# Kernel tuning notes

Measured on AMD Instinct MI355X. Metric: run time of the kernel, lower is better.

Reference implementation:

```python
import jax, jax.numpy as jnp
import numpy as np

EMBED_DIM = 768
NUM_HEADS = 12
HEAD_DIM = EMBED_DIM // NUM_HEADS


def setup_inputs() -> dict:
    key = jax.random.key(0)
    ks = jax.random.split(key, 9)
    B, N, C = 4, 2048, EMBED_DIM
    s = 1.0 / np.sqrt(C)
    x = jax.random.normal(ks[0], (B, N, C), dtype=jnp.float32)
    Wq = jax.random.normal(ks[1], (C, C), dtype=jnp.float32) * s
    bq = jnp.zeros((C,), dtype=jnp.float32)
    Wk = jax.random.normal(ks[2], (C, C), dtype=jnp.float32) * s
    bk = jnp.zeros((C,), dtype=jnp.float32)
    Wv = jax.random.normal(ks[3], (C, C), dtype=jnp.float32) * s
    bv = jnp.zeros((C,), dtype=jnp.float32)
    Wo = jax.random.normal(ks[4], (C, C), dtype=jnp.float32) * s
    bo = jnp.zeros((C,), dtype=jnp.float32)
    return {"x": x, "Wq": Wq, "bq": bq, "Wk": Wk, "bk": bk,
            "Wv": Wv, "bv": bv, "Wo": Wo, "bo": bo}


def reference(x, Wq, bq, Wk, bk, Wv, bv, Wo, bo):
    # Dropout in eval mode (identity), matching module.eval().
    B, N, C = x.shape
    H, D = NUM_HEADS, HEAD_DIM
    scale = D ** -0.5

    def split_heads(t):  # [B,N,C] -> [B,H,N,D]
        return t.reshape(B, N, H, D).transpose(0, 2, 1, 3)

    q = split_heads(x @ Wq.T + bq)
    k = split_heads(x @ Wk.T + bk)
    v = split_heads(x @ Wv.T + bv)

    attn = jnp.einsum('bhnd,bhmd->bhnm', q, k) * scale  # [B,H,N,N]
    attn = jax.nn.softmax(attn, axis=-1)
    out = jnp.einsum('bhnm,bhmd->bhnd', attn, v)        # [B,H,N,D]
    out = out.transpose(0, 2, 1, 3).reshape(B, N, C)
    return out @ Wo.T + bo
```

## Files before the change

### kernel.cpp

```cpp
#include <hip/hip_runtime.h>
#include <math.h>

#define CDIM 768
#define NHEADS 12
#define HDIM 64
#define BATCH 4
#define SEQ 2048
#define MTOT (BATCH*SEQ)
#define NQKV (3*CDIM)
#define QROWS 128

typedef __attribute__((ext_vector_type(8))) short bf16x8;
typedef __attribute__((ext_vector_type(4))) float f32x4;
typedef unsigned short u16;

#define ASYNC16(gsrc, ldst) \
  __builtin_amdgcn_global_load_lds((const __attribute__((address_space(1))) void*)(gsrc), \
                                   (__attribute__((address_space(3))) void*)(ldst), 16, 0, 0)

__device__ inline u16 f2b(float x) {
    unsigned int u = __float_as_uint(x);
    return (u16)((u + 0x7fffu + ((u >> 16) & 1u)) >> 16);
}
__device__ inline u16 f2b_hu(float x) {
    return (u16)((__float_as_uint(x) + 0x8000u) >> 16);
}

__global__ void f2bf_kern(const float* __restrict__ in, u16* __restrict__ out, int n)
{
    int i = (blockIdx.x * 256 + threadIdx.x) * 4;
    if (i >= n) return;
    float4 v = *(const float4*)(in + i);
    ushort4 o;
    o.x = f2b(v.x); o.y = f2b(v.y); o.z = f2b(v.z); o.w = f2b(v.w);
    *(ushort4*)(out + i) = o;
}

__global__ void castw_kern(const float* __restrict__ Wq, const float* __restrict__ Wk,
                           const float* __restrict__ Wv, const float* __restrict__ Wo,
                           u16* __restrict__ wqkv, u16* __restrict__ wob)
{
    int z = blockIdx.y;
    const float* src = (z == 0) ? Wq : (z == 1) ? Wk : (z == 2) ? Wv : Wo;
    u16* dst = (z == 3) ? wob : wqkv + (size_t)z * CDIM * CDIM;
    int i = (blockIdx.x * 256 + threadIdx.x) * 4;
    float4 v = *(const float4*)(src + i);
    ushort4 o;
    o.x = f2b(v.x); o.y = f2b(v.y); o.z = f2b(v.z); o.w = f2b(v.w);
    *(ushort4*)(dst + i) = o;
}

__global__ void catbias_kern(const float* __restrict__ bq, const float* __restrict__ bk,
                             const float* __restrict__ bv, float* __restrict__ out)
{
    int i = blockIdx.x * 256 + threadIdx.x;
    if (i < CDIM) out[i] = bq[i];
    else if (i < 2*CDIM) out[i] = bk[i - CDIM];
    else if (i < 3*CDIM) out[i] = bv[i - 2*CDIM];
}

template<int OUTF32>
__global__ __launch_bounds__(256)
void gemm_bf16(const u16* __restrict__ A, const u16* __restrict__ B,
               const float* __restrict__ bias, void* __restrict__ Y,
               int N, int K, int qn, float qscale)
{
    __shared__ __align__(16) u16 As[128*64];
    __shared__ __align__(16) u16 Bs[128*64];
    const int tid = threadIdx.x;
    const int m0 = blockIdx.y * 128, n0 = blockIdx.x * 128;
    const int wid = tid >> 6, lane = tid & 63;
    const int wm = (wid & 1) * 64, wn = (wid >> 1) * 64;
    const int l15 = lane & 15, quad = lane >> 4;

    f32x4 acc[4][4];
    #pragma unroll
    for (int i = 0; i < 4; ++i)
        #pragma unroll
        for (int j = 0; j < 4; ++j)
            #pragma unroll
            for (int r = 0; r < 4; ++r) acc[i][j][r] = 0.f;

    for (int k0 = 0; k0 < K; k0 += 64) {
        __syncthreads();
        #pragma unroll
        for (int r = 0; r < 4; ++r) {
            int li = r*256 + tid;
            int row = li >> 3, c = li & 7;
            int gc = c ^ (row & 7);
            ASYNC16(A + (size_t)(m0 + row) * K + k0 + gc*8, &As[li*8]);
            ASYNC16(B + (size_t)(n0 + row) * K + k0 + gc*8, &Bs[li*8]);
        }
        __syncthreads();
        #pragma unroll
        for (int kk = 0; kk < 2; ++kk) {
            bf16x8 a[4], b[4];
            #pragma unroll
            for (int i = 0; i < 4; ++i) {
                int m = wm + i*16 + l15;
                int ca = (kk*4 + quad) ^ (m & 7);
                a[i] = *(const bf16x8*)&As[m*64 + ca*8];
                int n = wn + i*16 + l15;
                int cb = (kk*4 + quad) ^ (n & 7);
                b[i] = *(const bf16x8*)&Bs[n*64 + cb*8];
            }
            #pragma unroll
            for (int i = 0; i < 4; ++i)
                #pragma unroll
                for (int j = 0; j < 4; ++j)
                    acc[i][j] = __builtin_amdgcn_mfma_f32_16x16x32_bf16(a[i], b[j], acc[i][j], 0, 0, 0);
        }
    }

    #pragma unroll
    for (int i = 0; i < 4; ++i) {
        #pragma unroll
        for (int j = 0; j < 4; ++j) {
            int gn = n0 + wn + j*16 + l15;
            float bv = bias[gn];
            float sc = (gn < qn) ? qscale : 1.0f;
            #pragma unroll
            for (int r = 0; r < 4; ++r) {
                int gm = m0 + wm + i*16 + quad*4 + r;
                float v = (acc[i][j][r] + bv) * sc;
                if (OUTF32) ((float*)Y)[(size_t)gm * N + gn] = v;
                else        ((u16*)Y)[(size_t)gm * N + gn] = f2b(v);
            }
        }
    }
}

__global__ __launch_bounds__(256)
void transpose_v(const u16* __restrict__ QKV, u16* __restrict__ Vt)
{
    __shared__ __align__(16) u16 Vs[64*72];
    const int tid = threadIdx.x;
    const int nt = blockIdx.x, bh = blockIdx.y;
    const int b = bh / NHEADS, h = bh % NHEADS;
    const u16* src = QKV + ((size_t)(b*SEQ + nt*64)) * NQKV + 2*CDIM + h*HDIM;
    #pragma unroll
    for (int rep = 0; rep < 2; ++rep) {
        int li = rep*256 + tid, r = li >> 3, c = li & 7;
        *(uint4*)&Vs[r*72 + c*8] = *(const uint4*)(src + (size_t)r * NQKV + c*8);
    }
    __syncthreads();
    u16* dst = Vt + ((size_t)bh * 64) * SEQ + nt*64;
    #pragma unroll
    for (int rep = 0; rep < 2; ++rep) {
        int li = rep*256 + tid, d = li >> 3, c = li & 7;
        u16 tmp[8];
        #pragma unroll
        for (int j = 0; j < 8; ++j) tmp[j] = Vs[(c*8 + j)*72 + d];
        *(uint4*)(dst + (size_t)d * SEQ + c*8) = *(const uint4*)tmp;
    }
}

__global__ __launch_bounds__(256, 3)
void attn_mfma(const u16* __restrict__ QK, const u16* __restrict__ Vt,
               u16* __restrict__ Oa)
{
    __shared__ __align__(16) u16 Ps[QROWS*72];
    __shared__ __align__(16) u16 Ks[2][64*64];
    __shared__ __align__(16) u16 Vs[2][64*64];

    const int tid = threadIdx.x;
    const int wid = tid >> 6, lane = tid & 63;
    const int l15 = lane & 15, quad = lane >> 4;
    const int qt = blockIdx.x, bh = blockIdx.y;
    const int b = bh / NHEADS, h = bh % NHEADS;

    const u16* Qg  = QK + ((size_t)(b*SEQ + qt*QROWS)) * NQKV + h*HDIM;
    const u16* Kg0 = QK + ((size_t)(b*SEQ)) * NQKV + CDIM + h*HDIM;
    const u16* Vg0 = Vt + (size_t)bh * HDIM * SEQ;

    #pragma unroll
    for (int r = 0; r < 4; ++r) {
        int li = r*256 + tid, row = li >> 3, c = li & 7, gc = c ^ (row & 7);
        ASYNC16(Qg + (size_t)row * NQKV + gc*8, &Ps[li*8]);
    }
    #pragma unroll
    for (int r = 0; r < 2; ++r) {
        int li = r*256 + tid, row = li >> 3, c = li & 7, gc = c ^ (row & 7);
        ASYNC16(Kg0 + (size_t)row * NQKV + gc*8, &Ks[0][li*8]);
        ASYNC16(Vg0 + (size_t)row * SEQ + gc*8, &Vs[0][li*8]);
    }
    __syncthreads();

    bf16x8 qf[2][2];
    #pragma unroll
    for (int mb = 0; mb < 2; ++mb)
        #pragma unroll
        for (int kk = 0; kk < 2; ++kk) {
            int m = wid*32 + mb*16 + l15;
            int c = (kk*4 + quad) ^ (m & 7);
            qf[mb][kk] = *(const bf16x8*)&Ps[m*64 + c*8];
        }
    __syncthreads();

    f32x4 o[2][4];
    #pragma unroll
    for (int mb = 0; mb < 2; ++mb)
        #pragma unroll
        for (int j = 0; j < 4; ++j)
            #pragma unroll
            for (int r = 0; r < 4; ++r) o[mb][j][r] = 0.f;
    float l_run[2][4] = {};

    for (int kt = 0; kt < SEQ/64; ++kt) {
        const int cb = kt & 1, nb = cb ^ 1;
        if (kt + 1 < SEQ/64) {
            #pragma unroll
            for (int r = 0; r < 2; ++r) {
                int li = r*256 + tid, row = li >> 3, c = li & 7, gc = c ^ (row & 7);
                ASYNC16(Kg0 + (size_t)((kt+1)*64 + row) * NQKV + gc*8, &Ks[nb][li*8]);
                ASYNC16(Vg0 + (size_t)row * SEQ + (kt+1)*64 + gc*8, &Vs[nb][li*8]);
            }
        }

        f32x4 s[2][4];
        #pragma unroll
        for (int mb = 0; mb < 2; ++mb)
            #pragma unroll
            for (int j = 0; j < 4; ++j)
                #pragma unroll
                for (int r = 0; r < 4; ++r) s[mb][j][r] = 0.f;
        #pragma unroll
        for (int kk = 0; kk < 2; ++kk) {
            bf16x8 bk[4];
            #pragma unroll
            for (int j = 0; j < 4; ++j) {
                int nk = j*16 + l15;
                int ck = (kk*4 + quad) ^ (nk & 7);
                bk[j] = *(const bf16x8*)&Ks[cb][nk*64 + ck*8];
            }
            #pragma unroll
            for (int mb = 0; mb < 2; ++mb)
                #pragma unroll
                for (int j = 0; j < 4; ++j)
                    s[mb][j] = __builtin_amdgcn_mfma_f32_16x16x32_bf16(qf[mb][kk], bk[j], s[mb][j], 0, 0, 0);
        }

        #pragma unroll
        for (int mb = 0; mb < 2; ++mb)
            #pragma unroll
            for (int j = 0; j < 4; ++j)
                #pragma unroll
                for (int r = 0; r < 4; ++r) {
                    float p = __expf(s[mb][j][r]);
                    l_run[mb][r] += p;
                    Ps[(wid*32 + mb*16 + quad*4 + r)*72 + j*16 + l15] = f2b_hu(p);
                }

        #pragma unroll
        for (int kk = 0; kk < 2; ++kk) {
            bf16x8 bv[4];
            #pragma unroll
            for (int j = 0; j < 4; ++j) {
                int nd = j*16 + l15;
                int cv = (kk*4 + quad) ^ (nd & 7);
                bv[j] = *(const bf16x8*)&Vs[cb][nd*64 + cv*8];
            }
            #pragma unroll
            for (int mb = 0; mb < 2; ++mb) {
                bf16x8 ap = *(const bf16x8*)&Ps[(wid*32 + mb*16 + l15)*72 + (kk*4 + quad)*8];
                #pragma unroll
                for (int j = 0; j < 4; ++j)
                    o[mb][j] = __builtin_amdgcn_mfma_f32_16x16x32_bf16(ap, bv[j], o[mb][j], 0, 0, 0);
            }
        }
        __syncthreads();
    }

    u16* Og = Oa + ((size_t)(b*SEQ + qt*QROWS)) * CDIM + h*HDIM;
    #pragma unroll
    for (int mb = 0; mb < 2; ++mb)
        #pragma unroll
        for (int r = 0; r < 4; ++r) {
            float l = l_run[mb][r];
            #pragma unroll
            for (int off = 1; off < 16; off <<= 1)
                l += __shfl_xor(l, off);
            float inv = 1.f / l;
            int row = wid*32 + mb*16 + quad*4 + r;
            #pragma unroll
            for (int j = 0; j < 4; ++j)
                Og[(size_t)row * CDIM + j*16 + l15] = f2b(o[mb][j][r] * inv);
        }
}

extern "C" void kernel_launch(void* const* d_in, const int* in_sizes, int n_in,
                              void* d_out, int out_size, void* d_ws, size_t ws_size,
                              hipStream_t stream)
{
    const float* x  = (const float*)d_in[0];
    const float* Wq = (const float*)d_in[1];
    const float* bq = (const float*)d_in[2];
    const float* Wk = (const float*)d_in[3];
    const float* bk = (const float*)d_in[4];
    const float* Wv = (const float*)d_in[5];
    const float* bv = (const float*)d_in[6];
    const float* Wo = (const float*)d_in[7];
    const float* bo = (const float*)d_in[8];

    unsigned char* ws = (unsigned char*)d_ws;
    u16* xb   = (u16*)ws;  ws += (size_t)MTOT * CDIM * 2;
    u16* wqkv = (u16*)ws;  ws += (size_t)NQKV * CDIM * 2;
    u16* wob  = (u16*)ws;  ws += (size_t)CDIM * CDIM * 2;
    float* bcat = (float*)ws; ws += (size_t)NQKV * 4;
    u16* qkv  = (u16*)ws;  ws += (size_t)MTOT * NQKV * 2;
    u16* vt   = (u16*)ws;  ws += (size_t)BATCH*NHEADS*HDIM*SEQ * 2;
    u16* ao   = (u16*)ws;

    f2bf_kern<<<MTOT*CDIM/1024, 256, 0, stream>>>(x, xb, MTOT*CDIM);
    castw_kern<<<dim3(CDIM*CDIM/1024, 4), 256, 0, stream>>>(Wq, Wk, Wv, Wo, wqkv, wob);
    catbias_kern<<<(NQKV+255)/256, 256, 0, stream>>>(bq, bk, bv, bcat);

    gemm_bf16<0><<<dim3(NQKV/128, MTOT/128), 256, 0, stream>>>(xb, wqkv, bcat, qkv, NQKV, CDIM, CDIM, 0.125f);
    transpose_v<<<dim3(SEQ/64, BATCH*NHEADS), 256, 0, stream>>>(qkv, vt);
    attn_mfma<<<dim3(SEQ/QROWS, BATCH*NHEADS), 256, 0, stream>>>(qkv, vt, ao);
    gemm_bf16<1><<<dim3(CDIM/128, MTOT/128), 256, 0, stream>>>(ao, wob, bo, (float*)d_out, CDIM, CDIM, 0, 1.0f);
}
```

Measured before the change: 251.8 us.

## Keep attention probabilities in registers via transposed QK^T MFMA

The score MFMA is computed as K·Q^T so each lane's accumulator layout matches the A-operand of a 16x16x16 bf16 MFMA. The exponentiated probabilities are then packed into bf16x4 fragments directly, with no round-trip through the shared Ps buffer. The row sums come from an extra MFMA against a ones vector, which replaces the per-lane accumulation and cross-lane shuffles. exp is replaced by exp2 with log2e folded into the Q scale, Q is loaded directly from global memory, and the Ps shared array is removed, freeing LDS for occupancy. The cost is a smaller-K MFMA for PV and narrower 8-byte V reads from LDS.

```diff
diff --git a/kernel.cpp b/kernel.cpp
--- a/kernel.cpp
+++ b/kernel.cpp
@@ -11,8 +11,10 @@
 #define QROWS 128
 
 typedef __attribute__((ext_vector_type(8))) short bf16x8;
+typedef __attribute__((ext_vector_type(4))) short bf16x4;
 typedef __attribute__((ext_vector_type(4))) float f32x4;
 typedef unsigned short u16;
+typedef unsigned int u32;
 
 #define ASYNC16(gsrc, ldst) \
   __builtin_amdgcn_global_load_lds((const __attribute__((address_space(1))) void*)(gsrc), \
@@ -22,9 +24,7 @@
     unsigned int u = __float_as_uint(x);
     return (u16)((u + 0x7fffu + ((u >> 16) & 1u)) >> 16);
 }
-__device__ inline u16 f2b_hu(float x) {
-    return (u16)((__float_as_uint(x) + 0x8000u) >> 16);
-}
+__device__ inline u32 prnd(float x) { return __float_as_uint(x) + 0x8000u; }
 
 __global__ void f2bf_kern(const float* __restrict__ in, u16* __restrict__ out, int n)
 {
@@ -159,7 +159,6 @@
 void attn_mfma(const u16* __restrict__ QK, const u16* __restrict__ Vt,
                u16* __restrict__ Oa)
 {
-    __shared__ __align__(16) u16 Ps[QROWS*72];
     __shared__ __align__(16) u16 Ks[2][64*64];
     __shared__ __align__(16) u16 Vs[2][64*64];
 
@@ -174,37 +173,34 @@
     const u16* Vg0 = Vt + (size_t)bh * HDIM * SEQ;
 
     #pragma unroll
-    for (int r = 0; r < 4; ++r) {
-        int li = r*256 + tid, row = li >> 3, c = li & 7, gc = c ^ (row & 7);
-        ASYNC16(Qg + (size_t)row * NQKV + gc*8, &Ps[li*8]);
-    }
-    #pragma unroll
     for (int r = 0; r < 2; ++r) {
         int li = r*256 + tid, row = li >> 3, c = li & 7, gc = c ^ (row & 7);
         ASYNC16(Kg0 + (size_t)row * NQKV + gc*8, &Ks[0][li*8]);
         ASYNC16(Vg0 + (size_t)row * SEQ + gc*8, &Vs[0][li*8]);
     }
+    bf16x8 qf[2][2];
+    #pragma unroll
+    for (int mb = 0; mb < 2; ++mb)
+        #pragma unroll
+        for (int kk = 0; kk < 2; ++kk)
+            qf[mb][kk] = *(const bf16x8*)(Qg + (size_t)(wid*32 + mb*16 + l15) * NQKV + kk*32 + quad*8);
+
+    const bf16x4 ONES = { (short)0x3F80, (short)0x3F80, (short)0x3F80, (short)0x3F80 };
+
+    f32x4 o[2][4];
+    #pragma unroll
+    for (int mb = 0; mb < 2; ++mb)
+        #pragma unroll
+        for (int j = 0; j < 4; ++j)
+            #pragma unroll
+            for (int r = 0; r < 4; ++r) o[mb][j][r] = 0.f;
+    f32x4 ll[2];
+    #pragma unroll
+    for (int mb = 0; mb < 2; ++mb)
+        #pragma unroll
+        for (int r = 0; r < 4; ++r) ll[mb][r] = 0.f;
+
     __syncthreads();
-
-    bf16x8 qf[2][2];
-    #pragma unroll
-    for (int mb = 0; mb < 2; ++mb)
-        #pragma unroll
-        for (int kk = 0; kk < 2; ++kk) {
-            int m = wid*32 + mb*16 + l15;
-            int c = (kk*4 + quad) ^ (m & 7);
-            qf[mb][kk] = *(const bf16x8*)&Ps[m*64 + c*8];
-        }
-    __syncthreads();
-
-    f32x4 o[2][4];
-    #pragma unroll
-    for (int mb = 0; mb < 2; ++mb)
-        #pragma unroll
-        for (int j = 0; j < 4; ++j)
-            #pragma unroll
-            for (int r = 0; r < 4; ++r) o[mb][j][r] = 0.f;
-    float l_run[2][4] = {};
 
     for (int kt = 0; kt < SEQ/64; ++kt) {
         const int cb = kt & 1, nb = cb ^ 1;
@@ -226,66 +222,62 @@
                 for (int r = 0; r < 4; ++r) s[mb][j][r] = 0.f;
         #pragma unroll
         for (int kk = 0; kk < 2; ++kk) {
-            bf16x8 bk[4];
             #pragma unroll
             for (int j = 0; j < 4; ++j) {
-                int nk = j*16 + l15;
-                int ck = (kk*4 + quad) ^ (nk & 7);
-                bk[j] = *(const bf16x8*)&Ks[cb][nk*64 + ck*8];
+                int kr = j*16 + l15;
+                int ck = (kk*4 + quad) ^ (kr & 7);
+                bf16x8 ak = *(const bf16x8*)&Ks[cb][kr*64 + ck*8];
+                #pragma unroll
+                for (int mb = 0; mb < 2; ++mb)
+                    s[mb][j] = __builtin_amdgcn_mfma_f32_16x16x32_bf16(ak, qf[mb][kk], s[mb][j], 0, 0, 0);
+            }
+        }
+
+        bf16x4 pf[2][4];
+        #pragma unroll
+        for (int mb = 0; mb < 2; ++mb)
+            #pragma unroll
+            for (int ks = 0; ks < 4; ++ks) {
+                u32 u0 = prnd(__builtin_amdgcn_exp2f(s[mb][ks][0]));
+                u32 u1 = prnd(__builtin_amdgcn_exp2f(s[mb][ks][1]));
+                u32 u2 = prnd(__builtin_amdgcn_exp2f(s[mb][ks][2]));
+                u32 u3 = prnd(__builtin_amdgcn_exp2f(s[mb][ks][3]));
+                union { uint2 u; bf16x4 v; } cst;
+                cst.u.x = __builtin_amdgcn_perm(u1, u0, 0x07060302u);
+                cst.u.y = __builtin_amdgcn_perm(u3, u2, 0x07060302u);
+                pf[mb][ks] = cst.v;
+            }
+
+        #pragma unroll
+        for (int ks = 0; ks < 4; ++ks) {
+            int seqoff = ks*16 + quad*4;
+            int chunk = (seqoff >> 3) ^ (l15 & 7);
+            #pragma unroll
+            for (int jd = 0; jd < 4; ++jd) {
+                bf16x4 vv = *(const bf16x4*)&Vs[cb][(jd*16 + l15)*64 + chunk*8 + (seqoff & 7)];
+                #pragma unroll
+                for (int mb = 0; mb < 2; ++mb)
+                    o[mb][jd] = __builtin_amdgcn_mfma_f32_16x16x16bf16_1k(pf[mb][ks], vv, o[mb][jd], 0, 0, 0);
             }
             #pragma unroll
             for (int mb = 0; mb < 2; ++mb)
-                #pragma unroll
-                for (int j = 0; j < 4; ++j)
-                    s[mb][j] = __builtin_amdgcn_mfma_f32_16x16x32_bf16(qf[mb][kk], bk[j], s[mb][j], 0, 0, 0);
-        }
-
-        #pragma unroll
-        for (int mb = 0; mb < 2; ++mb)
-            #pragma unroll
-            for (int j = 0; j < 4; ++j)
-                #pragma unroll
-                for (int r = 0; r < 4; ++r) {
-                    float p = __expf(s[mb][j][r]);
-                    l_run[mb][r] += p;
-                    Ps[(wid*32 + mb*16 + quad*4 + r)*72 + j*16 + l15] = f2b_hu(p);
-                }
-
-        #pragma unroll
-        for (int kk = 0; kk < 2; ++kk) {
-            bf16x8 bv[4];
-            #pragma unroll
-            for (int j = 0; j < 4; ++j) {
-                int nd = j*16 + l15;
-                int cv = (kk*4 + quad) ^ (nd & 7);
-                bv[j] = *(const bf16x8*)&Vs[cb][nd*64 + cv*8];
-            }
-            #pragma unroll
-            for (int mb = 0; mb < 2; ++mb) {
-                bf16x8 ap = *(const bf16x8*)&Ps[(wid*32 + mb*16 + l15)*72 + (kk*4 + quad)*8];
-                #pragma unroll
-                for (int j = 0; j < 4; ++j)
-                    o[mb][j] = __builtin_amdgcn_mfma_f32_16x16x32_bf16(ap, bv[j], o[mb][j], 0, 0, 0);
-            }
+                ll[mb] = __builtin_amdgcn_mfma_f32_16x16x16bf16_1k(pf[mb][ks], ONES, ll[mb], 0, 0, 0);
         }
         __syncthreads();
     }
 
     u16* Og = Oa + ((size_t)(b*SEQ + qt*QROWS)) * CDIM + h*HDIM;
     #pragma unroll
-    for (int mb = 0; mb < 2; ++mb)
+    for (int mb = 0; mb < 2; ++mb) {
         #pragma unroll
         for (int r = 0; r < 4; ++r) {
-            float l = l_run[mb][r];
-            #pragma unroll
-            for (int off = 1; off < 16; off <<= 1)
-                l += __shfl_xor(l, off);
-            float inv = 1.f / l;
+            float inv = 1.f / ll[mb][r];
             int row = wid*32 + mb*16 + quad*4 + r;
             #pragma unroll
-            for (int j = 0; j < 4; ++j)
-                Og[(size_t)row * CDIM + j*16 + l15] = f2b(o[mb][j][r] * inv);
-        }
+            for (int jd = 0; jd < 4; ++jd)
+                Og[(size_t)row * CDIM + jd*16 + l15] = f2b(o[mb][jd][r] * inv);
+        }
+    }
 }
 
 extern "C" void kernel_launch(void* const* d_in, const int* in_sizes, int n_in,
@@ -315,7 +307,7 @@
     castw_kern<<<dim3(CDIM*CDIM/1024, 4), 256, 0, stream>>>(Wq, Wk, Wv, Wo, wqkv, wob);
     catbias_kern<<<(NQKV+255)/256, 256, 0, stream>>>(bq, bk, bv, bcat);
 
-    gemm_bf16<0><<<dim3(NQKV/128, MTOT/128), 256, 0, stream>>>(xb, wqkv, bcat, qkv, NQKV, CDIM, CDIM, 0.125f);
+    gemm_bf16<0><<<dim3(NQKV/128, MTOT/128), 256, 0, stream>>>(xb, wqkv, bcat, qkv, NQKV, CDIM, CDIM, 0.18033688f);
     transpose_v<<<dim3(SEQ/64, BATCH*NHEADS), 256, 0, stream>>>(qkv, vt);
     attn_mfma<<<dim3(SEQ/QROWS, BATCH*NHEADS), 256, 0, stream>>>(qkv, vt, ao);
     gemm_bf16<1><<<dim3(CDIM/128, MTOT/128), 256, 0, stream>>>(ao, wob, bo, (float*)d_out, CDIM, CDIM, 0, 1.0f);
```

Result: faster. 242.9 us (-3.5%).
